# Optimization experiments

Measured on AMD Instinct MI355X. Metric: run time of the kernel, lower is better.

The kernel has to match this reference:

```python
import jax, jax.numpy as jnp
import numpy as np

N_NODES = 100000
N_EDGES = 6400000
N_GRAPHS = 1000
D_IN = 16
D_HID = 16
D_OUT = 6


def setup_inputs() -> dict:
    key = jax.random.key(0)
    ks = jax.random.split(key, 12)
    x = jax.random.normal(ks[0], (N_NODES, D_IN), dtype=jnp.float32)
    edge_index = jax.random.randint(ks[1], (2, N_EDGES), 0, N_NODES, dtype=jnp.int64)
    edge_attr = jax.random.normal(ks[2], (N_EDGES, D_IN), dtype=jnp.float32)
    batch = jnp.sort(jax.random.randint(ks[3], (N_NODES,), 0, N_GRAPHS, dtype=jnp.int64))
    s = 1.0 / np.sqrt(D_HID)
    W1a = jax.random.uniform(ks[4], (D_IN, D_HID), jnp.float32, -s, s)
    b1a = jax.random.uniform(ks[5], (D_HID,), jnp.float32, -s, s)
    W1b = jax.random.uniform(ks[6], (D_HID, D_HID), jnp.float32, -s, s)
    b1b = jax.random.uniform(ks[7], (D_HID,), jnp.float32, -s, s)
    W2a = jax.random.uniform(ks[8], (D_HID, D_OUT), jnp.float32, -s, s)
    b2a = jax.random.uniform(ks[9], (D_OUT,), jnp.float32, -s, s)
    W2b = jax.random.uniform(ks[10], (D_OUT, D_OUT), jnp.float32, -s, s)
    b2b = jax.random.uniform(ks[11], (D_OUT,), jnp.float32, -s, s)
    return {"x": x, "edge_index": edge_index, "edge_attr": edge_attr, "batch": batch,
            "W1a": W1a, "b1a": b1a, "W1b": W1b, "b1b": b1b,
            "W2a": W2a, "b2a": b2a, "W2b": W2b, "b2b": b2b}


def _gine_conv(x, edge_index, edge_attr, mlp):
    # message: relu(x_j + e), aggregated by sum at target node; eps = 0
    src, dst = edge_index[0], edge_index[1]
    msg = jax.nn.relu(x[src] + edge_attr)                       # [E, D]
    aggr = jax.ops.segment_sum(msg, dst, num_segments=N_NODES)  # [N, D]
    return mlp(x + aggr)


def reference(x, edge_index, edge_attr, batch,
              W1a, b1a, W1b, b1b, W2a, b2a, W2b, b2b):
    mlp1 = lambda h: jax.nn.relu(h @ W1a + b1a) @ W1b + b1b
    mlp2 = lambda h: jax.nn.relu(h @ W2a + b2a) @ W2b + b2b
    h = _gine_conv(x, edge_index, edge_attr, mlp1)
    h = jax.nn.relu(h)  # dropout is identity in eval mode
    h = _gine_conv(h, edge_index, edge_attr, mlp2)
    # global mean pool over graphs
    sums = jax.ops.segment_sum(h, batch, num_segments=N_GRAPHS)          # [G, D_OUT]
    counts = jax.ops.segment_sum(jnp.ones((N_NODES,), h.dtype), batch,
                                 num_segments=N_GRAPHS)
    pooled = sums / jnp.maximum(counts, 1.0)[:, None]
    return jax.nn.log_softmax(pooled, axis=1)
```

## Files before the change

kernel.cpp:

```cpp
#include <hip/hip_runtime.h>
#include <math.h>

#define N_NODES  100000
#define N_EDGES  6400000
#define N_GRAPHS 1000
#define D_IN  16
#define D_HID 16
#define D_OUT 6

#define B_NODES   64
#define NBUCK     ((N_NODES + B_NODES - 1) / B_NODES)
#define CAPB      4608
#define NSLOTS    ((size_t)NBUCK * CAPB)
#define EPB       16384
#define KBLOCKS   ((N_EDGES + EPB - 1) / EPB)

__global__ __launch_bounds__(1024) void scatter_direct(
    const int* __restrict__ ei, int* __restrict__ cnt, int2* __restrict__ tmp)
{
    __shared__ int hist[NBUCK];
    __shared__ int base[NBUCK];
    int t = threadIdx.x;
    for (int i = t; i < NBUCK; i += 1024) hist[i] = 0;
    __syncthreads();
    int e0 = blockIdx.x * EPB;
#pragma unroll
    for (int k = 0; k < EPB / 1024; ++k) {
        int e = e0 + k * 1024 + t;
        if (e < N_EDGES) atomicAdd(&hist[ei[N_EDGES + e] >> 6], 1);
    }
    __syncthreads();
    for (int i = t; i < NBUCK; i += 1024) {
        int h = hist[i];
        base[i] = h ? atomicAdd(&cnt[i], h) : 0;
        hist[i] = 0;
    }
    __syncthreads();
#pragma unroll
    for (int k = 0; k < EPB / 1024; ++k) {
        int e = e0 + k * 1024 + t;
        if (e < N_EDGES) {
            int dst = ei[N_EDGES + e];
            int src = ei[e];
            int b = dst >> 6;
            int r = base[b] + atomicAdd(&hist[b], 1);
            if (r < CAPB)
                tmp[(size_t)b * CAPB + r] = make_int2(((dst & 63) << 23) | e, src);
        }
    }
}

__global__ __launch_bounds__(1024) void bucket_place(
    const int* __restrict__ cnt, const int2* __restrict__ tmp,
    int2* __restrict__ csr, int2* __restrict__ offs2)
{
    __shared__ int2 stage[CAPB];
    __shared__ int hist[B_NODES];
    int b = blockIdx.x, t = threadIdx.x;
    int m = cnt[b];
    if (m > CAPB) m = CAPB;
    int beg = b * CAPB;
    for (int i = t; i < m; i += 1024) stage[i] = tmp[beg + i];
    if (t < B_NODES) hist[t] = 0;
    __syncthreads();
    for (int i = t; i < m; i += 1024)
        atomicAdd(&hist[(stage[i].x >> 23) & 63], 1);
    __syncthreads();
    if (t < 64) {
        int v = hist[t], sc = v;
#pragma unroll
        for (int d = 1; d < 64; d <<= 1) {
            int o = __shfl_up(sc, d, 64);
            if (t >= d) sc += o;
        }
        int ex = sc - v;
        int node = b * 64 + t;
        if (node < N_NODES) offs2[node] = make_int2(beg + ex, beg + ex + v);
        hist[t] = ex;
    }
    __syncthreads();
    for (int i = t; i < m; i += 1024) {
        int2 p = stage[i];
        int d = (p.x >> 23) & 63;
        int e = p.x & 0x7FFFFF;
        int r = atomicAdd(&hist[d], 1);
        csr[beg + r] = make_int2(p.y, e);
    }
}

__global__ __launch_bounds__(256) void gather1_mlp(
    const int2* __restrict__ offs2, const int2* __restrict__ csr,
    const float* __restrict__ x, const float* __restrict__ eattr,
    const float* __restrict__ W1a, const float* __restrict__ b1a,
    const float* __restrict__ W1b, const float* __restrict__ b1b,
    float* __restrict__ h)
{
    __shared__ float sWa[256], sWb[256], sba[16], sbb[16];
    __shared__ float sV[16][17];
    int t = threadIdx.x;
    sWa[t] = W1a[t]; sWb[t] = W1b[t];
    if (t < 16) { sba[t] = b1a[t]; sbb[t] = b1b[t]; }

    int lane = t & 15, grp = t >> 4;
    int n = blockIdx.x * 16 + grp;
    int2 oo = offs2[n];
    int i = oo.x, end = oo.y;
    float acc = 0.0f;
    for (; i + 12 <= end; i += 12) {
        int2 p[12];
#pragma unroll
        for (int k = 0; k < 12; ++k) p[k] = csr[i + k];
        float ev[12];
#pragma unroll
        for (int k = 0; k < 12; ++k)
            ev[k] = __builtin_nontemporal_load(eattr + (size_t)p[k].y * 16 + lane);
        float fv[12];
#pragma unroll
        for (int k = 0; k < 12; ++k)
            fv[k] = x[(size_t)p[k].x * 16 + lane];
#pragma unroll
        for (int k = 0; k < 12; ++k)
            acc += fmaxf(ev[k] + fv[k], 0.0f);
    }
    for (; i < end; ++i) {
        int2 p = csr[i];
        acc += fmaxf(__builtin_nontemporal_load(eattr + (size_t)p.y * 16 + lane)
                     + x[(size_t)p.x * 16 + lane], 0.0f);
    }

    sV[grp][lane] = x[(size_t)n * 16 + lane] + acc;
    __syncthreads();
    float s = sba[lane];
#pragma unroll
    for (int ii = 0; ii < 16; ++ii) s += sV[grp][ii] * sWa[ii * 16 + lane];
    float u = fmaxf(s, 0.0f);
    __syncthreads();
    sV[grp][lane] = u;
    __syncthreads();
    float s2 = sbb[lane];
#pragma unroll
    for (int ii = 0; ii < 16; ++ii) s2 += sV[grp][ii] * sWb[ii * 16 + lane];
    h[(size_t)n * 16 + lane] = fmaxf(s2, 0.0f);
}

__global__ __launch_bounds__(256) void gather2_mlp(
    const int2* __restrict__ offs2, const int2* __restrict__ csr,
    const float* __restrict__ hfeat, const float* __restrict__ eattr,
    const int* __restrict__ batch,
    const float* __restrict__ W2a, const float* __restrict__ b2a,
    const float* __restrict__ W2b, const float* __restrict__ b2b,
    float* __restrict__ sums)
{
    __shared__ float sWa[96], sWb[36], sba[6], sbb[6];
    __shared__ float sV[16][17];
    __shared__ float sO[16][6];
    __shared__ int   sGr[16];
    int t = threadIdx.x;
    if (t < 96) sWa[t] = W2a[t];
    if (t < 36) sWb[t] = W2b[t];
    if (t < 6)  { sba[t] = b2a[t]; sbb[t] = b2b[t]; }

    int lane = t & 15, grp = t >> 4;
    int n = blockIdx.x * 16 + grp;
    int2 oo = offs2[n];
    int i = oo.x, end = oo.y;
    float acc = 0.0f;
    for (; i + 12 <= end; i += 12) {
        int2 p[12];
#pragma unroll
        for (int k = 0; k < 12; ++k) p[k] = csr[i + k];
        float ev[12];
#pragma unroll
        for (int k = 0; k < 12; ++k)
            ev[k] = __builtin_nontemporal_load(eattr + (size_t)p[k].y * 16 + lane);
        float fv[12];
#pragma unroll
        for (int k = 0; k < 12; ++k)
            fv[k] = hfeat[(size_t)p[k].x * 16 + lane];
#pragma unroll
        for (int k = 0; k < 12; ++k)
            acc += fmaxf(ev[k] + fv[k], 0.0f);
    }
    for (; i < end; ++i) {
        int2 p = csr[i];
        acc += fmaxf(__builtin_nontemporal_load(eattr + (size_t)p.y * 16 + lane)
                     + hfeat[(size_t)p.x * 16 + lane], 0.0f);
    }

    sV[grp][lane] = hfeat[(size_t)n * 16 + lane] + acc;
    __syncthreads();
    float u = 0.0f;
    if (lane < 6) {
        float s = sba[lane];
#pragma unroll
        for (int ii = 0; ii < 16; ++ii) s += sV[grp][ii] * sWa[ii * 6 + lane];
        u = fmaxf(s, 0.0f);
    }
    __syncthreads();
    sV[grp][lane] = u;
    __syncthreads();
    if (lane < 6) {
        float s2 = sbb[lane];
#pragma unroll
        for (int ii = 0; ii < 6; ++ii) s2 += sV[grp][ii] * sWb[ii * 6 + lane];
        sO[grp][lane] = s2;
    }
    if (lane == 0) sGr[grp] = batch[n];
    __syncthreads();

    if (t < 6) {
        float run = sO[0][t];
        int curg = sGr[0];
        for (int q = 1; q < 16; ++q) {
            int g = sGr[q];
            if (g == curg) run += sO[q][t];
            else { atomicAdd(&sums[(size_t)curg * 6 + t], run); curg = g; run = sO[q][t]; }
        }
        atomicAdd(&sums[(size_t)curg * 6 + t], run);
    }
}

__device__ __forceinline__ int lower_bound(const int* __restrict__ a, int n, int key)
{
    int lo = 0, hi = n;
    while (lo < hi) { int mid = (lo + hi) >> 1; if (a[mid] < key) lo = mid + 1; else hi = mid; }
    return lo;
}

__global__ __launch_bounds__(256) void pool_kernel(
    const float* __restrict__ sums, const int* __restrict__ batch,
    float* __restrict__ out)
{
    int g = blockIdx.x * blockDim.x + threadIdx.x;
    if (g >= N_GRAPHS) return;
    int c0 = lower_bound(batch, N_NODES, g);
    int c1 = lower_bound(batch, N_NODES, g + 1);
    float c = fmaxf((float)(c1 - c0), 1.0f);
    float p[6];
    float mx = -INFINITY;
#pragma unroll
    for (int j = 0; j < 6; ++j) {
        p[j] = sums[(size_t)g * 6 + j] / c;
        mx = fmaxf(mx, p[j]);
    }
    float se = 0.0f;
#pragma unroll
    for (int j = 0; j < 6; ++j) se += expf(p[j] - mx);
    float lse = mx + logf(se);
#pragma unroll
    for (int j = 0; j < 6; ++j) out[(size_t)g * 6 + j] = p[j] - lse;
}

extern "C" void kernel_launch(void* const* d_in, const int* in_sizes, int n_in,
                              void* d_out, int out_size, void* d_ws, size_t ws_size,
                              hipStream_t stream)
{
    const float* x     = (const float*)d_in[0];
    const int*   ei    = (const int*)  d_in[1];
    const float* eattr = (const float*)d_in[2];
    const int*   batch = (const int*)  d_in[3];
    const float* W1a = (const float*)d_in[4];
    const float* b1a = (const float*)d_in[5];
    const float* W1b = (const float*)d_in[6];
    const float* b1b = (const float*)d_in[7];
    const float* W2a = (const float*)d_in[8];
    const float* b2a = (const float*)d_in[9];
    const float* W2b = (const float*)d_in[10];
    const float* b2b = (const float*)d_in[11];
    float* out = (float*)d_out;

    int2*  tmp    = (int2*)d_ws;
    int2*  csr    = tmp + NSLOTS;
    float* h      = (float*)(csr + NSLOTS);
    int2*  offs2  = (int2*)(h + (size_t)N_NODES * 16);
    int*   cnt    = (int*)(offs2 + N_NODES);
    float* sums   = (float*)(cnt + NBUCK);

    const int TB = 256;
    const int g_blocks = N_NODES / 16;

    hipMemsetAsync(cnt, 0, (size_t)NBUCK * sizeof(int), stream);
    scatter_direct<<<KBLOCKS, 1024, 0, stream>>>(ei, cnt, tmp);
    bucket_place<<<NBUCK, 1024, 0, stream>>>(cnt, tmp, csr, offs2);

    gather1_mlp<<<g_blocks, TB, 0, stream>>>(offs2, csr, x, eattr,
                                             W1a, b1a, W1b, b1b, h);

    hipMemsetAsync(sums, 0, (size_t)(N_GRAPHS * 6) * sizeof(float), stream);
    gather2_mlp<<<g_blocks, TB, 0, stream>>>(offs2, csr, h, eattr, batch,
                                             W2a, b2a, W2b, b2b, sums);

    pool_kernel<<<(N_GRAPHS + TB - 1) / TB, TB, 0, stream>>>(sums, batch, out);
}
```

Baseline: 537.9 us.

## Single-pass bucket scatter with register-held ranks and 128-node buckets

The scatter kernel now reads the edge index once, using int2 vector loads, and keeps the per-edge local ranks from the first histogram pass in registers. This removes the second global read and the second shared atomic pass. The bucket placement kernel drops its shared staging array and holds entries and ranks in registers. It uses 128-node buckets with a two-wave prefix scan, so there are fewer, larger buckets and more blocks in flight. This raises register pressure and adds some capacity risk, because bucket capacity is a fixed constant that silently drops overflow.

```diff
diff --git a/kernel.cpp b/kernel.cpp
--- a/kernel.cpp
+++ b/kernel.cpp
@@ -8,44 +8,58 @@
 #define D_HID 16
 #define D_OUT 6
 
-#define B_NODES   64
+#define B_NODES   128
 #define NBUCK     ((N_NODES + B_NODES - 1) / B_NODES)
-#define CAPB      4608
+#define CAPB      8960
 #define NSLOTS    ((size_t)NBUCK * CAPB)
-#define EPB       16384
+#define EPB       8192
 #define KBLOCKS   ((N_EDGES + EPB - 1) / EPB)
 
-__global__ __launch_bounds__(1024) void scatter_direct(
+__global__ __launch_bounds__(512) void scatter_direct(
     const int* __restrict__ ei, int* __restrict__ cnt, int2* __restrict__ tmp)
 {
     __shared__ int hist[NBUCK];
     __shared__ int base[NBUCK];
     int t = threadIdx.x;
-    for (int i = t; i < NBUCK; i += 1024) hist[i] = 0;
+    for (int i = t; i < NBUCK; i += 512) hist[i] = 0;
     __syncthreads();
     int e0 = blockIdx.x * EPB;
-#pragma unroll
-    for (int k = 0; k < EPB / 1024; ++k) {
-        int e = e0 + k * 1024 + t;
-        if (e < N_EDGES) atomicAdd(&hist[ei[N_EDGES + e] >> 6], 1);
-    }
-    __syncthreads();
-    for (int i = t; i < NBUCK; i += 1024) {
+
+    int2 d2[8], s2[8];
+    int rnk0[8], rnk1[8];
+#pragma unroll
+    for (int k = 0; k < 8; ++k) {
+        int e = e0 + k * 1024 + 2 * t;
+        if (e < N_EDGES) {
+            d2[k] = *(const int2*)(ei + N_EDGES + e);
+            s2[k] = *(const int2*)(ei + e);
+            rnk0[k] = atomicAdd(&hist[d2[k].x >> 7], 1);
+            rnk1[k] = atomicAdd(&hist[d2[k].y >> 7], 1);
+        } else {
+            d2[k].x = -1; d2[k].y = -1; s2[k].x = s2[k].y = 0;
+            rnk0[k] = rnk1[k] = 0;
+        }
+    }
+    __syncthreads();
+    for (int i = t; i < NBUCK; i += 512) {
         int h = hist[i];
         base[i] = h ? atomicAdd(&cnt[i], h) : 0;
-        hist[i] = 0;
-    }
-    __syncthreads();
-#pragma unroll
-    for (int k = 0; k < EPB / 1024; ++k) {
-        int e = e0 + k * 1024 + t;
-        if (e < N_EDGES) {
-            int dst = ei[N_EDGES + e];
-            int src = ei[e];
-            int b = dst >> 6;
-            int r = base[b] + atomicAdd(&hist[b], 1);
-            if (r < CAPB)
-                tmp[(size_t)b * CAPB + r] = make_int2(((dst & 63) << 23) | e, src);
+    }
+    __syncthreads();
+#pragma unroll
+    for (int k = 0; k < 8; ++k) {
+        int e = e0 + k * 1024 + 2 * t;
+        if (d2[k].x >= 0) {
+            int b0 = d2[k].x >> 7;
+            int r0 = base[b0] + rnk0[k];
+            if (r0 < CAPB)
+                tmp[(size_t)b0 * CAPB + r0] =
+                    make_int2(((d2[k].x & 127) << 23) | e, s2[k].x);
+            int b1 = d2[k].y >> 7;
+            int r1 = base[b1] + rnk1[k];
+            if (r1 < CAPB)
+                tmp[(size_t)b1 * CAPB + r1] =
+                    make_int2(((d2[k].y & 127) << 23) | (e + 1), s2[k].y);
         }
     }
 }
@@ -54,37 +68,55 @@
     const int* __restrict__ cnt, const int2* __restrict__ tmp,
     int2* __restrict__ csr, int2* __restrict__ offs2)
 {
-    __shared__ int2 stage[CAPB];
     __shared__ int hist[B_NODES];
+    __shared__ int wtot;
     int b = blockIdx.x, t = threadIdx.x;
     int m = cnt[b];
     if (m > CAPB) m = CAPB;
     int beg = b * CAPB;
-    for (int i = t; i < m; i += 1024) stage[i] = tmp[beg + i];
     if (t < B_NODES) hist[t] = 0;
     __syncthreads();
-    for (int i = t; i < m; i += 1024)
-        atomicAdd(&hist[(stage[i].x >> 23) & 63], 1);
-    __syncthreads();
-    if (t < 64) {
-        int v = hist[t], sc = v;
+
+    int2 p[9];
+    int rnk[9];
+#pragma unroll
+    for (int j = 0; j < 9; ++j) {
+        int i = t + j * 1024;
+        if (i < m) {
+            p[j] = tmp[beg + i];
+            rnk[j] = atomicAdd(&hist[(p[j].x >> 23) & 127], 1);
+        } else { p[j].x = -1; p[j].y = 0; rnk[j] = 0; }
+    }
+    __syncthreads();
+
+    int v = 0, sc = 0;
+    if (t < B_NODES) {
+        v = hist[t];
+        sc = v;
 #pragma unroll
         for (int d = 1; d < 64; d <<= 1) {
             int o = __shfl_up(sc, d, 64);
-            if (t >= d) sc += o;
-        }
+            if ((t & 63) >= d) sc += o;
+        }
+        if (t == 63) wtot = sc;
+    }
+    __syncthreads();
+    if (t < B_NODES) {
+        if (t >= 64) sc += wtot;
         int ex = sc - v;
-        int node = b * 64 + t;
+        int node = b * B_NODES + t;
         if (node < N_NODES) offs2[node] = make_int2(beg + ex, beg + ex + v);
         hist[t] = ex;
     }
     __syncthreads();
-    for (int i = t; i < m; i += 1024) {
-        int2 p = stage[i];
-        int d = (p.x >> 23) & 63;
-        int e = p.x & 0x7FFFFF;
-        int r = atomicAdd(&hist[d], 1);
-        csr[beg + r] = make_int2(p.y, e);
+
+#pragma unroll
+    for (int j = 0; j < 9; ++j) {
+        if (p[j].x >= 0) {
+            int d = (p[j].x >> 23) & 127;
+            int e = p[j].x & 0x7FFFFF;
+            csr[beg + hist[d] + rnk[j]] = make_int2(p[j].y, e);
+        }
     }
 }
 
@@ -280,13 +312,13 @@
     const int g_blocks = N_NODES / 16;
 
     hipMemsetAsync(cnt, 0, (size_t)NBUCK * sizeof(int), stream);
-    scatter_direct<<<KBLOCKS, 1024, 0, stream>>>(ei, cnt, tmp);
+    hipMemsetAsync(sums, 0, (size_t)(N_GRAPHS * 6) * sizeof(float), stream);
+    scatter_direct<<<KBLOCKS, 512, 0, stream>>>(ei, cnt, tmp);
     bucket_place<<<NBUCK, 1024, 0, stream>>>(cnt, tmp, csr, offs2);
 
     gather1_mlp<<<g_blocks, TB, 0, stream>>>(offs2, csr, x, eattr,
                                              W1a, b1a, W1b, b1b, h);
 
-    hipMemsetAsync(sums, 0, (size_t)(N_GRAPHS * 6) * sizeof(float), stream);
     gather2_mlp<<<g_blocks, TB, 0, stream>>>(offs2, csr, h, eattr, batch,
                                              W2a, b2a, W2b, b2b, sums);
 
```

Result: slower. 550.9 us (+2.4%).
